# Performance work log

Hardware: AMD Instinct MI355X
Metric: run time of the kernel (lower is better)

Reference implementation:

```python
import jax, jax.numpy as jnp
import numpy as np

B, S, P, D, H = 2, 4096, 1024, 1024, 16  # batch, byte seq, patches, d_model, heads


def setup_inputs() -> dict:
    key = jax.random.key(0)
    ks = jax.random.split(key, 8)
    init = 0.02
    queries = jax.random.normal(ks[0], (B, S, D), dtype=jnp.float32)
    patch_representations = jax.random.normal(ks[1], (B, P, D), dtype=jnp.float32)
    patch_boundaries = jax.random.randint(ks[2], (B, S), 0, 2, dtype=jnp.int32)
    wq = jax.random.normal(ks[3], (D, D), dtype=jnp.float32) * init
    wk = jax.random.normal(ks[4], (D, D), dtype=jnp.float32) * init
    wv = jax.random.normal(ks[5], (D, D), dtype=jnp.float32) * init
    wo = jax.random.normal(ks[6], (D, D), dtype=jnp.float32) * init
    bq = jnp.zeros((D,), jnp.float32)
    bk = jnp.zeros((D,), jnp.float32)
    bv = jnp.zeros((D,), jnp.float32)
    bo = jnp.zeros((D,), jnp.float32)
    return {"queries": queries, "patch_representations": patch_representations,
            "patch_boundaries": patch_boundaries,
            "wq": wq, "wk": wk, "wv": wv, "wo": wo,
            "bq": bq, "bk": bk, "bv": bv, "bo": bo}


def reference(queries, patch_representations, patch_boundaries,
              wq, wk, wv, wo, bq, bk, bv, bo):
    b, s, d = queries.shape
    p = patch_representations.shape[1]
    h = H
    dh = d // h
    scale = 1.0 / jnp.sqrt(jnp.asarray(dh, queries.dtype))

    # in-projections (torch Linear: x @ W.T + b)
    q = (queries @ wq.T + bq).reshape(b, s, h, dh)
    k = (patch_representations @ wk.T + bk).reshape(b, p, h, dh)
    v = (patch_representations @ wv.T + bv).reshape(b, p, h, dh)

    # scores: [b, h, s, p]
    scores = jnp.einsum('bqhd,bkhd->bhqk', q, k) * scale

    # data-dependent patch-boundary mask: byte t may attend to patch j iff j <= cumsum(boundaries)[t]
    patch_idx = jnp.cumsum(patch_boundaries, axis=1)          # [b, s]
    mask = jnp.arange(p)[None, None, :] > patch_idx[:, :, None]  # [b, s, p], True = masked
    scores = jnp.where(mask[:, None, :, :], jnp.finfo(scores.dtype).min, scores)

    attn = jax.nn.softmax(scores, axis=-1)                    # dropout inactive (eval)
    out = jnp.einsum('bhqk,bkhd->bqhd', attn, v).reshape(b, s, d)
    return out @ wo.T + bo
```

## Files before the change

### kernel.cpp

```cpp
#include <hip/hip_runtime.h>


#define B_ 2
#define S_ 4096
#define P_ 1024
#define D_ 1024
#define H_ 16
#define DH_ 64

#define NCONV 14336

typedef __attribute__((ext_vector_type(8))) short short8;
typedef __attribute__((ext_vector_type(4))) float f32x4;
typedef __attribute__((ext_vector_type(16))) float f32x16;

#define KSCALE 0.18033688011112042f

#if __has_builtin(__builtin_amdgcn_exp2f)
#define EXP2(x) __builtin_amdgcn_exp2f(x)
#else
#define EXP2(x) exp2f(x)
#endif

static __device__ __forceinline__ unsigned short f2bf(float f) {
    unsigned int u = __float_as_uint(f);
    u += 0x7FFFu + ((u >> 16) & 1u);
    return (unsigned short)(u >> 16);
}

static __device__ __forceinline__ unsigned int cvtpk(float lo, float hi) {
    unsigned int r;
    asm("v_cvt_pk_bf16_f32 %0, %1, %2" : "=v"(r) : "v"(lo), "v"(hi));
    return r;
}

static __device__ __forceinline__ void plswap(unsigned int& x, unsigned int& y) {
    asm volatile("v_permlane32_swap_b32 %0, %1" : "+v"(x), "+v"(y));
}

static __device__ __forceinline__ void gll16(const unsigned short* g,
                                             const unsigned short* l) {
    __builtin_amdgcn_global_load_lds(
        (const __attribute__((address_space(1))) unsigned int*)g,
        (__attribute__((address_space(3))) unsigned int*)l,
        16, 0, 0);
}

__global__ __launch_bounds__(256) void xattn_convert_all(
    const float* __restrict__ queries, const float* __restrict__ patches,
    const float* __restrict__ wq, const float* __restrict__ wk,
    const float* __restrict__ wv, const float* __restrict__ wo,
    unsigned short* __restrict__ qb, unsigned short* __restrict__ pb,
    unsigned short* __restrict__ wqb, unsigned short* __restrict__ wkb,
    unsigned short* __restrict__ wvb, unsigned short* __restrict__ wob,
    const int* __restrict__ bounds, int* __restrict__ pidx) {
    if (blockIdx.x >= NCONV) {
        __shared__ int sdata[256];
        int b = blockIdx.x - NCONV;
        int t = threadIdx.x;
        const int* src = bounds + b * S_ + t * 16;
        int vals[16];
        int run = 0;
#pragma unroll
        for (int i = 0; i < 16; ++i) { run += src[i]; vals[i] = run; }
        sdata[t] = run;
        __syncthreads();
        for (int off = 1; off < 256; off <<= 1) {
            int v = (t >= off) ? sdata[t - off] : 0;
            __syncthreads();
            sdata[t] += v;
            __syncthreads();
        }
        int prefix = (t > 0) ? sdata[t - 1] : 0;
        int* dst = pidx + b * S_ + t * 16;
#pragma unroll
        for (int i = 0; i < 16; ++i) dst[i] = prefix + vals[i];
        return;
    }
    const int NQ = (B_ * S_ * D_) / 4;
    const int NP = (B_ * P_ * D_) / 4;
    const int NW = (D_ * D_) / 4;
    int i = blockIdx.x * 256 + threadIdx.x;
    const float* src;
    unsigned short* dst;
    int j;
    if (i < NQ) { src = queries; dst = qb; j = i; }
    else if (i < NQ + NP) { src = patches; dst = pb; j = i - NQ; }
    else {
        int k = i - NQ - NP;
        int wsel = k >> 18;
        j = k & (NW - 1);
        if (wsel == 0) { src = wq; dst = wqb; }
        else if (wsel == 1) { src = wk; dst = wkb; }
        else if (wsel == 2) { src = wv; dst = wvb; }
        else { src = wo; dst = wob; }
    }
    float4 v = ((const float4*)src)[j];
    ushort4 o;
    o.x = f2bf(v.x); o.y = f2bf(v.y); o.z = f2bf(v.z); o.w = f2bf(v.w);
    ((ushort4*)dst)[j] = o;
}

__global__ __launch_bounds__(512) void xattn_gemm_qkv(
    const unsigned short* __restrict__ qb, const unsigned short* __restrict__ pb,
    const unsigned short* __restrict__ wqb, const unsigned short* __restrict__ wkb,
    const unsigned short* __restrict__ wvb,
    const float* __restrict__ bq, const float* __restrict__ bk,
    const float* __restrict__ bv,
    unsigned short* __restrict__ Qout, unsigned short* __restrict__ Kout,
    unsigned short* __restrict__ Vout) {
    const int K = 1024, N = 1024;
    const int byy = blockIdx.y;
    int z, my;
    if (byy < 64)      { z = 0; my = byy; }
    else if (byy < 80) { z = 1; my = byy - 64; }
    else               { z = 2; my = byy - 80; }
    const unsigned short* A = (z == 0) ? qb : pb;
    const unsigned short* W = (z == 0) ? wqb : ((z == 1) ? wkb : wvb);
    const float* bias = (z == 0) ? bq : ((z == 1) ? bk : bv);

    __shared__ unsigned short As[2][128 * 32];
    __shared__ unsigned short Bs[2][256 * 32];

    const int m0 = my * 128;
    const int n0 = blockIdx.x * 256;
    const int t = threadIdx.x;
    const int w = t >> 6;
    const int l = t & 63;
    const int fr = l & 15, fq = l >> 4;
    const int wr = w >> 2, wc = w & 3;

    const int r0s = t >> 2;
    const int csw = ((t & 3) ^ ((t >> 3) & 3)) * 8;
    const unsigned short* Ap0 = A + (size_t)(m0 + r0s) * K + csw;
    const unsigned short* Wp0 = W + (size_t)(n0 + r0s) * K + csw;
    const unsigned short* Wp1 = W + (size_t)(n0 + 128 + r0s) * K + csw;

    const int gsw = (fq ^ ((fr >> 1) & 3)) * 8;

    f32x4 acc[4][4];
#pragma unroll
    for (int i = 0; i < 4; ++i)
#pragma unroll
        for (int j = 0; j < 4; ++j) acc[i][j] = (f32x4){0.f, 0.f, 0.f, 0.f};

    gll16(Ap0, &As[0][w * 512]);
    gll16(Wp0, &Bs[0][w * 512]);
    gll16(Wp1, &Bs[0][4096 + w * 512]);

    for (int kt = 0; kt < 32; ++kt) {
        __builtin_amdgcn_s_barrier();
        if (kt + 1 < 32) {
            const int nb = (kt + 1) & 1;
            const int ks = (kt + 1) * 32;
            gll16(Ap0 + ks, &As[nb][w * 512]);
            gll16(Wp0 + ks, &Bs[nb][w * 512]);
            gll16(Wp1 + ks, &Bs[nb][4096 + w * 512]);
            asm volatile("s_waitcnt vmcnt(3)" ::: "memory");
        } else {
            asm volatile("s_waitcnt vmcnt(0)" ::: "memory");
        }
        __builtin_amdgcn_sched_barrier(0);
        __builtin_amdgcn_s_barrier();

        const unsigned short* Ac = As[kt & 1];
        const unsigned short* Bc = Bs[kt & 1];
        short8 af[4], bf[4];
#pragma unroll
        for (int i = 0; i < 4; ++i)
            af[i] = *(const short8*)&Ac[(wr * 64 + i * 16 + fr) * 32 + gsw];
#pragma unroll
        for (int j = 0; j < 4; ++j)
            bf[j] = *(const short8*)&Bc[(wc * 64 + j * 16 + fr) * 32 + gsw];
        __builtin_amdgcn_s_setprio(1);
#pragma unroll
        for (int i = 0; i < 4; ++i)
#pragma unroll
            for (int j = 0; j < 4; ++j)
                acc[i][j] = __builtin_amdgcn_mfma_f32_16x16x32_bf16(af[i], bf[j], acc[i][j], 0, 0, 0);
        __builtin_amdgcn_s_setprio(0);
    }

#pragma unroll
    for (int j = 0; j < 4; ++j) {
        int n = n0 + wc * 64 + j * 16 + fr;
        float bvv = bias[n];
#pragma unroll
        for (int i = 0; i < 4; ++i) {
            int mbase = m0 + wr * 64 + i * 16 + fq * 4;
#pragma unroll
            for (int r = 0; r < 4; ++r) {
                float val = acc[i][j][r] + bvv;
                int m = mbase + r;
                if (z == 0) {
                    Qout[(size_t)m * N + n] = f2bf(val * KSCALE);
                } else if (z == 1) {
                    int bb = m >> 10, p = m & (P_ - 1);
                    int hh = n >> 6, k = n & 63;
                    size_t base = ((size_t)((bb * H_ + hh) * 16 + (p >> 6))) * 4096;
                    int off = (((p >> 5) & 1) * 4 + (k >> 4)) * 512 +
                              (((k >> 3) & 1) * 32 + (p & 31)) * 8 + (k & 7);
                    Kout[base + off] = f2bf(val);
                } else {
                    int bb = m >> 10, p = m & (P_ - 1);
                    int hh = n >> 6, d = n & 63;
                    size_t base = ((size_t)((bb * H_ + hh) * 16 + (p >> 6))) * 4096;
                    int off = ((d >> 5) * 4 + ((p >> 4) & 3)) * 512 +
                              ((((p >> 3) & 1) * 32) + (d & 31)) * 8 + (p & 7);
                    Vout[base + off] = f2bf(val);
                }
            }
        }
    }
}

__global__ __launch_bounds__(512) void xattn_gemm_o(
    const unsigned short* __restrict__ A,
    const unsigned short* __restrict__ W,
    const float* __restrict__ bias,
    float* __restrict__ Cout) {
    const int K = 1024, N = 1024;
    __shared__ unsigned short As[2][128 * 32];
    __shared__ unsigned short Bs[2][256 * 32];

    const int m0 = blockIdx.y * 128;
    const int n0 = blockIdx.x * 256;
    const int t = threadIdx.x;
    const int w = t >> 6;
    const int l = t & 63;
    const int fr = l & 15, fq = l >> 4;
    const int wr = w >> 2, wc = w & 3;

    const int r0s = t >> 2;
    const int csw = ((t & 3) ^ ((t >> 3) & 3)) * 8;
    const unsigned short* Ap0 = A + (size_t)(m0 + r0s) * K + csw;
    const unsigned short* Wp0 = W + (size_t)(n0 + r0s) * K + csw;
    const unsigned short* Wp1 = W + (size_t)(n0 + 128 + r0s) * K + csw;

    const int gsw = (fq ^ ((fr >> 1) & 3)) * 8;

    f32x4 acc[4][4];
#pragma unroll
    for (int i = 0; i < 4; ++i)
#pragma unroll
        for (int j = 0; j < 4; ++j) acc[i][j] = (f32x4){0.f, 0.f, 0.f, 0.f};

    gll16(Ap0, &As[0][w * 512]);
    gll16(Wp0, &Bs[0][w * 512]);
    gll16(Wp1, &Bs[0][4096 + w * 512]);

    for (int kt = 0; kt < 32; ++kt) {
        __builtin_amdgcn_s_barrier();
        if (kt + 1 < 32) {
            const int nb = (kt + 1) & 1;
            const int ks = (kt + 1) * 32;
            gll16(Ap0 + ks, &As[nb][w * 512]);
            gll16(Wp0 + ks, &Bs[nb][w * 512]);
            gll16(Wp1 + ks, &Bs[nb][4096 + w * 512]);
            asm volatile("s_waitcnt vmcnt(3)" ::: "memory");
        } else {
            asm volatile("s_waitcnt vmcnt(0)" ::: "memory");
        }
        __builtin_amdgcn_sched_barrier(0);
        __builtin_amdgcn_s_barrier();

        const unsigned short* Ac = As[kt & 1];
        const unsigned short* Bc = Bs[kt & 1];
        short8 af[4], bf[4];
#pragma unroll
        for (int i = 0; i < 4; ++i)
            af[i] = *(const short8*)&Ac[(wr * 64 + i * 16 + fr) * 32 + gsw];
#pragma unroll
        for (int j = 0; j < 4; ++j)
            bf[j] = *(const short8*)&Bc[(wc * 64 + j * 16 + fr) * 32 + gsw];
        __builtin_amdgcn_s_setprio(1);
#pragma unroll
        for (int i = 0; i < 4; ++i)
#pragma unroll
            for (int j = 0; j < 4; ++j)
                acc[i][j] = __builtin_amdgcn_mfma_f32_16x16x32_bf16(af[i], bf[j], acc[i][j], 0, 0, 0);
        __builtin_amdgcn_s_setprio(0);
    }

#pragma unroll
    for (int j = 0; j < 4; ++j) {
        int n = n0 + wc * 64 + j * 16 + fr;
        float bvv = bias[n];
#pragma unroll
        for (int i = 0; i < 4; ++i) {
            int mbase = m0 + wr * 64 + i * 16 + fq * 4;
#pragma unroll
            for (int r = 0; r < 4; ++r)
                Cout[(size_t)(mbase + r) * N + n] = acc[i][j][r] + bvv;
        }
    }
}

__global__ __launch_bounds__(256) void xattn_attn_mfma(
    const unsigned short* __restrict__ Qb,
    const unsigned short* __restrict__ Kf,
    const unsigned short* __restrict__ Vf,
    const int* __restrict__ pidx,
    unsigned short* __restrict__ Ob) {
    __shared__ unsigned short Ks[2][4096];
    __shared__ unsigned short Vs[2][4096];

    const int q0 = (31 - blockIdx.x) * 128;
    const int h = blockIdx.y;
    const int b = blockIdx.z;
    const int t = threadIdx.x;
    const int w = t >> 6, l = t & 63;
    const int lq = l & 31, lh = l >> 5;
    const int qw = q0 + w * 32;

    const unsigned short* qrow =
        Qb + (size_t)(b * S_ + qw + lq) * D_ + h * DH_ + lh * 8;
    short8 qf[4];
#pragma unroll
    for (int ks = 0; ks < 4; ++ks) qf[ks] = *(const short8*)(qrow + ks * 16);

    const int prow = pidx[b * S_ + qw + lq];
    const int limit = pidx[b * S_ + q0 + 127];
    const int ntiles = (min(limit, P_ - 1) + 64) >> 6;
    const int nfull = (pidx[b * S_ + q0] + 1) >> 6;

    float l4[4] = {0.f, 0.f, 0.f, 0.f};
    f32x16 oacc[2] = {{}, {}};

    const unsigned short* kfb =
        Kf + (size_t)((b * H_ + h) * 16) * 4096 + (2 * w) * 512 + l * 8;
    const unsigned short* vfb =
        Vf + (size_t)((b * H_ + h) * 16) * 4096 + (2 * w) * 512 + l * 8;

    gll16(kfb, &Ks[0][(2 * w) * 512]);
    gll16(kfb + 512, &Ks[0][(2 * w + 1) * 512]);
    gll16(vfb, &Vs[0][(2 * w) * 512]);
    gll16(vfb + 512, &Vs[0][(2 * w + 1) * 512]);

    for (int kt = 0; kt < ntiles; ++kt) {
        __builtin_amdgcn_s_barrier();
        if (kt + 1 < ntiles) {
            const int nb = (kt + 1) & 1;
            const unsigned short* kn = kfb + (size_t)(kt + 1) * 4096;
            const unsigned short* vn = vfb + (size_t)(kt + 1) * 4096;
            gll16(kn, &Ks[nb][(2 * w) * 512]);
            gll16(kn + 512, &Ks[nb][(2 * w + 1) * 512]);
            gll16(vn, &Vs[nb][(2 * w) * 512]);
            gll16(vn + 512, &Vs[nb][(2 * w + 1) * 512]);
            asm volatile("s_waitcnt vmcnt(4)" ::: "memory");
        } else {
            asm volatile("s_waitcnt vmcnt(0)" ::: "memory");
        }
        __builtin_amdgcn_sched_barrier(0);
        __builtin_amdgcn_s_barrier();

        const unsigned short* Kc = Ks[kt & 1];
        const unsigned short* Vc = Vs[kt & 1];
        const int c0 = kt * 64;

        f32x16 sa[2];
        __builtin_amdgcn_s_setprio(1);
#pragma unroll
        for (int at = 0; at < 2; ++at) {
            f32x16 a = {};
#pragma unroll
            for (int ks = 0; ks < 4; ++ks) {
                short8 kfr = *(const short8*)&Kc[(at * 4 + ks) * 512 + l * 8];
                a = __builtin_amdgcn_mfma_f32_32x32x16_bf16(kfr, qf[ks], a, 0, 0, 0);
            }
            sa[at] = a;
        }
        __builtin_amdgcn_s_setprio(0);

        if (kt >= nfull) {
#pragma unroll
            for (int at = 0; at < 2; ++at)
#pragma unroll
                for (int r = 0; r < 16; ++r) {
                    const int pg = c0 + at * 32 + (r & 3) + 8 * (r >> 2) + 4 * lh;
                    float p = EXP2(sa[at][r]);
                    p = (pg > prow) ? 0.f : p;
                    sa[at][r] = p;
                    l4[r & 3] += p;
                }
        } else {
#pragma unroll
            for (int at = 0; at < 2; ++at)
#pragma unroll
                for (int r = 0; r < 16; ++r) {
                    float p = EXP2(sa[at][r]);
                    sa[at][r] = p;
                    l4[r & 3] += p;
                }
        }

        short8 pa[4];
#pragma unroll
        for (int ps = 0; ps < 4; ++ps) {
            const int pt = ps >> 1;
            const int rA = (ps & 1) * 8;
            unsigned int X0 = cvtpk(sa[pt][rA + 0], sa[pt][rA + 1]);
            unsigned int Y0 = cvtpk(sa[pt][rA + 4], sa[pt][rA + 5]);
            unsigned int X1 = cvtpk(sa[pt][rA + 2], sa[pt][rA + 3]);
            unsigned int Y1 = cvtpk(sa[pt][rA + 6], sa[pt][rA + 7]);
            plswap(X0, Y0);
            plswap(X1, Y1);
            uint4 u = {X0, X1, Y0, Y1};
            pa[ps] = *(short8*)&u;
        }

        __builtin_amdgcn_s_setprio(1);
#pragma unroll
        for (int dt = 0; dt < 2; ++dt)
#pragma unroll
            for (int ps = 0; ps < 4; ++ps) {
                short8 vfr = *(const short8*)&Vc[(dt * 4 + ps) * 512 + l * 8];
                oacc[dt] = __builtin_amdgcn_mfma_f32_32x32x16_bf16(pa[ps], vfr, oacc[dt], 0, 0, 0);
            }
        __builtin_amdgcn_s_setprio(0);
    }

    float lsum = (l4[0] + l4[1]) + (l4[2] + l4[3]);
    lsum += __shfl_xor(lsum, 32);
    const float inv = 1.0f / lsum;

    unsigned short* ob = Ob + (size_t)(b * S_ + qw) * D_ + h * DH_;
#pragma unroll
    for (int r = 0; r < 16; ++r) {
        const int qr = (r & 3) + 8 * (r >> 2) + 4 * lh;
        const float invr = __shfl(inv, qr);
        ob[(size_t)qr * D_ + lq] = f2bf(oacc[0][r] * invr);
        ob[(size_t)qr * D_ + 32 + lq] = f2bf(oacc[1][r] * invr);
    }
}

extern "C" void kernel_launch(void* const* d_in, const int* in_sizes, int n_in,
                              void* d_out, int out_size, void* d_ws, size_t ws_size,
                              hipStream_t stream) {
    const float* queries = (const float*)d_in[0];
    const float* patches = (const float*)d_in[1];
    const int* bounds    = (const int*)d_in[2];
    const float* wq = (const float*)d_in[3];
    const float* wk = (const float*)d_in[4];
    const float* wv = (const float*)d_in[5];
    const float* wo = (const float*)d_in[6];
    const float* bq = (const float*)d_in[7];
    const float* bk = (const float*)d_in[8];
    const float* bv = (const float*)d_in[9];
    const float* bo = (const float*)d_in[10];
    float* out = (float*)d_out;

    char* ws = (char*)d_ws;
    unsigned short* qb    = (unsigned short*)(ws + 0);
    unsigned short* pb    = (unsigned short*)(ws + 16777216);
    unsigned short* wqb   = (unsigned short*)(ws + 20971520);
    unsigned short* wkb   = (unsigned short*)(ws + 23068672);
    unsigned short* wvb   = (unsigned short*)(ws + 25165824);
    unsigned short* wob   = (unsigned short*)(ws + 27262976);
    unsigned short* Qbf   = (unsigned short*)(ws + 29360128);
    unsigned short* Kfr   = (unsigned short*)(ws + 46137344);
    unsigned short* Vfr   = (unsigned short*)(ws + 50331648);
    unsigned short* attnb = (unsigned short*)(ws + 54525952);
    int* pidx             = (int*)(ws + 71303168);

    xattn_convert_all<<<dim3(NCONV + B_), 256, 0, stream>>>(
        queries, patches, wq, wk, wv, wo, qb, pb, wqb, wkb, wvb, wob,
        bounds, pidx);
    xattn_gemm_qkv<<<dim3(4, 96), 512, 0, stream>>>(
        qb, pb, wqb, wkb, wvb, bq, bk, bv, Qbf, Kfr, Vfr);
    xattn_attn_mfma<<<dim3(S_ / 128, H_, B_), 256, 0, stream>>>(
        Qbf, Kfr, Vfr, pidx, attnb);
    xattn_gemm_o<<<dim3(4, 64), 512, 0, stream>>>(attnb, wob, bo, out);
}
```

Before: 236.5 us.

## Split each attention K/V tile across two wave groups and reduce through LDS

The attention kernel grows from 256 to 512 threads. Each pair of waves sharing a 32-query strip now handles half of every 64-key tile (one 32-key half each), instead of one wave doing the whole tile. The partial output accumulators and row sums are combined through shared memory at the end, and the K/V staging loads are spread over all eight waves. The goal is more waves per block to hide latency and halve per-wave serial MFMA/exp work, at the cost of extra barriers and an LDS reduction epilogue.

Measured after the change: 469.1 us. 98.3% more time.

```diff
diff --git a/kernel.cpp b/kernel.cpp
--- a/kernel.cpp
+++ b/kernel.cpp
@@ -296,7 +296,7 @@
     }
 }
 
-__global__ __launch_bounds__(256) void xattn_attn_mfma(
+__global__ __launch_bounds__(512, 6) void xattn_attn_mfma(
     const unsigned short* __restrict__ Qb,
     const unsigned short* __restrict__ Kf,
     const unsigned short* __restrict__ Vf,
@@ -311,7 +311,8 @@
     const int t = threadIdx.x;
     const int w = t >> 6, l = t & 63;
     const int lq = l & 31, lh = l >> 5;
-    const int qw = q0 + w * 32;
+    const int wq4 = w & 3, role = w >> 2;
+    const int qw = q0 + wq4 * 32;
 
     const unsigned short* qrow =
         Qb + (size_t)(b * S_ + qw + lq) * D_ + h * DH_ + lh * 8;
@@ -328,26 +329,20 @@
     f32x16 oacc[2] = {{}, {}};
 
     const unsigned short* kfb =
-        Kf + (size_t)((b * H_ + h) * 16) * 4096 + (2 * w) * 512 + l * 8;
+        Kf + (size_t)((b * H_ + h) * 16) * 4096 + w * 512 + l * 8;
     const unsigned short* vfb =
-        Vf + (size_t)((b * H_ + h) * 16) * 4096 + (2 * w) * 512 + l * 8;
-
-    gll16(kfb, &Ks[0][(2 * w) * 512]);
-    gll16(kfb + 512, &Ks[0][(2 * w + 1) * 512]);
-    gll16(vfb, &Vs[0][(2 * w) * 512]);
-    gll16(vfb + 512, &Vs[0][(2 * w + 1) * 512]);
+        Vf + (size_t)((b * H_ + h) * 16) * 4096 + w * 512 + l * 8;
+
+    gll16(kfb, &Ks[0][w * 512]);
+    gll16(vfb, &Vs[0][w * 512]);
 
     for (int kt = 0; kt < ntiles; ++kt) {
         __builtin_amdgcn_s_barrier();
         if (kt + 1 < ntiles) {
             const int nb = (kt + 1) & 1;
-            const unsigned short* kn = kfb + (size_t)(kt + 1) * 4096;
-            const unsigned short* vn = vfb + (size_t)(kt + 1) * 4096;
-            gll16(kn, &Ks[nb][(2 * w) * 512]);
-            gll16(kn + 512, &Ks[nb][(2 * w + 1) * 512]);
-            gll16(vn, &Vs[nb][(2 * w) * 512]);
-            gll16(vn + 512, &Vs[nb][(2 * w + 1) * 512]);
-            asm volatile("s_waitcnt vmcnt(4)" ::: "memory");
+            gll16(kfb + (size_t)(kt + 1) * 4096, &Ks[nb][w * 512]);
+            gll16(vfb + (size_t)(kt + 1) * 4096, &Vs[nb][w * 512]);
+            asm volatile("s_waitcnt vmcnt(2)" ::: "memory");
         } else {
             asm volatile("s_waitcnt vmcnt(0)" ::: "memory");
         }
@@ -358,79 +353,97 @@
         const unsigned short* Vc = Vs[kt & 1];
         const int c0 = kt * 64;
 
-        f32x16 sa[2];
+        f32x16 sa = {};
         __builtin_amdgcn_s_setprio(1);
 #pragma unroll
-        for (int at = 0; at < 2; ++at) {
-            f32x16 a = {};
-#pragma unroll
-            for (int ks = 0; ks < 4; ++ks) {
-                short8 kfr = *(const short8*)&Kc[(at * 4 + ks) * 512 + l * 8];
-                a = __builtin_amdgcn_mfma_f32_32x32x16_bf16(kfr, qf[ks], a, 0, 0, 0);
+        for (int ks = 0; ks < 4; ++ks) {
+            short8 kfr = *(const short8*)&Kc[(role * 4 + ks) * 512 + l * 8];
+            sa = __builtin_amdgcn_mfma_f32_32x32x16_bf16(kfr, qf[ks], sa, 0, 0, 0);
+        }
+        __builtin_amdgcn_s_setprio(0);
+
+        if (kt >= nfull) {
+#pragma unroll
+            for (int r = 0; r < 16; ++r) {
+                const int pg = c0 + role * 32 + (r & 3) + 8 * (r >> 2) + 4 * lh;
+                float p = EXP2(sa[r]);
+                p = (pg > prow) ? 0.f : p;
+                sa[r] = p;
+                l4[r & 3] += p;
             }
-            sa[at] = a;
-        }
-        __builtin_amdgcn_s_setprio(0);
-
-        if (kt >= nfull) {
-#pragma unroll
-            for (int at = 0; at < 2; ++at)
-#pragma unroll
-                for (int r = 0; r < 16; ++r) {
-                    const int pg = c0 + at * 32 + (r & 3) + 8 * (r >> 2) + 4 * lh;
-                    float p = EXP2(sa[at][r]);
-                    p = (pg > prow) ? 0.f : p;
-                    sa[at][r] = p;
-                    l4[r & 3] += p;
-                }
         } else {
 #pragma unroll
-            for (int at = 0; at < 2; ++at)
-#pragma unroll
-                for (int r = 0; r < 16; ++r) {
-                    float p = EXP2(sa[at][r]);
-                    sa[at][r] = p;
-                    l4[r & 3] += p;
-                }
-        }
-
-        short8 pa[4];
-#pragma unroll
-        for (int ps = 0; ps < 4; ++ps) {
-            const int pt = ps >> 1;
-            const int rA = (ps & 1) * 8;
-            unsigned int X0 = cvtpk(sa[pt][rA + 0], sa[pt][rA + 1]);
-            unsigned int Y0 = cvtpk(sa[pt][rA + 4], sa[pt][rA + 5]);
-            unsigned int X1 = cvtpk(sa[pt][rA + 2], sa[pt][rA + 3]);
-            unsigned int Y1 = cvtpk(sa[pt][rA + 6], sa[pt][rA + 7]);
+            for (int r = 0; r < 16; ++r) {
+                float p = EXP2(sa[r]);
+                sa[r] = p;
+                l4[r & 3] += p;
+            }
+        }
+
+        short8 pa[2];
+#pragma unroll
+        for (int psl = 0; psl < 2; ++psl) {
+            const int rA = psl * 8;
+            unsigned int X0 = cvtpk(sa[rA + 0], sa[rA + 1]);
+            unsigned int Y0 = cvtpk(sa[rA + 4], sa[rA + 5]);
+            unsigned int X1 = cvtpk(sa[rA + 2], sa[rA + 3]);
+            unsigned int Y1 = cvtpk(sa[rA + 6], sa[rA + 7]);
             plswap(X0, Y0);
             plswap(X1, Y1);
             uint4 u = {X0, X1, Y0, Y1};
-            pa[ps] = *(short8*)&u;
+            pa[psl] = *(short8*)&u;
         }
 
         __builtin_amdgcn_s_setprio(1);
 #pragma unroll
         for (int dt = 0; dt < 2; ++dt)
 #pragma unroll
-            for (int ps = 0; ps < 4; ++ps) {
-                short8 vfr = *(const short8*)&Vc[(dt * 4 + ps) * 512 + l * 8];
-                oacc[dt] = __builtin_amdgcn_mfma_f32_32x32x16_bf16(pa[ps], vfr, oacc[dt], 0, 0, 0);
+            for (int psl = 0; psl < 2; ++psl) {
+                short8 vfr = *(const short8*)
+                    &Vc[(dt * 4 + role * 2 + psl) * 512 + l * 8];
+                oacc[dt] = __builtin_amdgcn_mfma_f32_32x32x16_bf16(pa[psl], vfr, oacc[dt], 0, 0, 0);
             }
         __builtin_amdgcn_s_setprio(0);
     }
 
     float lsum = (l4[0] + l4[1]) + (l4[2] + l4[3]);
-    lsum += __shfl_xor(lsum, 32);
-    const float inv = 1.0f / lsum;
-
-    unsigned short* ob = Ob + (size_t)(b * S_ + qw) * D_ + h * DH_;
-#pragma unroll
-    for (int r = 0; r < 16; ++r) {
-        const int qr = (r & 3) + 8 * (r >> 2) + 4 * lh;
-        const float invr = __shfl(inv, qr);
-        ob[(size_t)qr * D_ + lq] = f2bf(oacc[0][r] * invr);
-        ob[(size_t)qr * D_ + 32 + lq] = f2bf(oacc[1][r] * invr);
+    float* cf = (float*)&Ks[0][0];
+    float* lf = (float*)&Vs[0][0];
+    const int ci = wq4 * 64 + l;
+
+    __builtin_amdgcn_s_barrier();
+    if (role) {
+#pragma unroll
+        for (int r = 0; r < 16; ++r) cf[ci * 16 + r] = oacc[0][r];
+        lf[ci] = lsum;
+    }
+    __builtin_amdgcn_s_barrier();
+    if (!role) {
+#pragma unroll
+        for (int r = 0; r < 16; ++r) oacc[0][r] += cf[ci * 16 + r];
+        lsum += lf[ci];
+    }
+    __builtin_amdgcn_s_barrier();
+    if (role) {
+#pragma unroll
+        for (int r = 0; r < 16; ++r) cf[ci * 16 + r] = oacc[1][r];
+    }
+    __builtin_amdgcn_s_barrier();
+    if (!role) {
+#pragma unroll
+        for (int r = 0; r < 16; ++r) oacc[1][r] += cf[ci * 16 + r];
+
+        lsum += __shfl_xor(lsum, 32);
+        const float inv = 1.0f / lsum;
+
+        unsigned short* ob = Ob + (size_t)(b * S_ + qw) * D_ + h * DH_;
+#pragma unroll
+        for (int r = 0; r < 16; ++r) {
+            const int qr = (r & 3) + 8 * (r >> 2) + 4 * lh;
+            const float invr = __shfl(inv, qr);
+            ob[(size_t)qr * D_ + lq] = f2bf(oacc[0][r] * invr);
+            ob[(size_t)qr * D_ + 32 + lq] = f2bf(oacc[1][r] * invr);
+        }
     }
 }
 
@@ -468,7 +481,7 @@
         bounds, pidx);
     xattn_gemm_qkv<<<dim3(4, 96), 512, 0, stream>>>(
         qb, pb, wqb, wkb, wvb, bq, bk, bv, Qbf, Kfr, Vfr);
-    xattn_attn_mfma<<<dim3(S_ / 128, H_, B_), 256, 0, stream>>>(
+    xattn_attn_mfma<<<dim3(S_ / 128, H_, B_), 512, 0, stream>>>(
         Qbf, Kfr, Vfr, pidx, attnb);
     xattn_gemm_o<<<dim3(4, 64), 512, 0, stream>>>(attnb, wob, bo, out);
 }
```
